# Optimization experiments

Measured on AMD Instinct MI355X. Metric: run time of the kernel, lower is better.

Reference implementation:

```python
import jax, jax.numpy as jnp
import numpy as np
from jax import lax

B, T, H, L, V = 64, 512, 1024, 4, 32000


def setup_inputs() -> dict:
    key = jax.random.key(0)
    ks = jax.random.split(key, 8)
    lengths = jax.random.randint(ks[0], (B,), T // 2, T + 1)
    tok = jax.random.randint(ks[1], (B, T), 1, V)  # valid tokens are >0; 0 is pad
    x = jnp.where(jnp.arange(T)[None, :] < lengths[:, None], tok, 0)
    s = float(1.0 / np.sqrt(H))  # torch LSTMCell default init bound
    emb = jax.random.normal(ks[2], (V, H), jnp.float32) * 0.02
    W_ih = jax.random.uniform(ks[3], (L, 4 * H, H), jnp.float32, -s, s)
    W_hh = jax.random.uniform(ks[4], (L, 4 * H, H), jnp.float32, -s, s)
    b_ih = jax.random.uniform(ks[5], (L, 4 * H), jnp.float32, -s, s)
    b_hh = jax.random.uniform(ks[6], (L, 4 * H), jnp.float32, -s, s)
    h0 = jnp.zeros((L, B, H), jnp.float32)
    c0 = jnp.zeros((L, B, H), jnp.float32)
    return {"x": x, "h0": h0, "c0": c0, "emb": emb,
            "W_ih": W_ih, "W_hh": W_hh, "b_ih": b_ih, "b_hh": b_hh}


def _lstm_stack_step(h, c, xt, W_ih, W_hh, b_ih, b_hh):
    # h, c: [L, B, H]; xt: [B, H]. Every layer is H->H (module quirk).
    inp = xt
    new_h, new_c = [], []
    for l in range(L):
        gates = inp @ W_ih[l].T + b_ih[l] + h[l] @ W_hh[l].T + b_hh[l]  # [B, 4H]
        i, f, g, o = jnp.split(gates, 4, axis=-1)  # torch gate order i,f,g,o
        i = jax.nn.sigmoid(i)
        f = jax.nn.sigmoid(f)
        g = jnp.tanh(g)
        o = jax.nn.sigmoid(o)
        cl = f * c[l] + i * g
        hl = o * jnp.tanh(cl)
        new_h.append(hl)
        new_c.append(cl)
        inp = hl
    return jnp.stack(new_h), jnp.stack(new_c)


def reference(x, h0, c0, emb, W_ih, W_hh, b_ih, b_hh):
    # lengths from pad-token convention (pad id = 0)
    lengths = jnp.sum(x > 0, axis=1)  # [B]
    # pack(..., enforce_sorted=False): sort sequences by length, descending.
    order = jnp.argsort(-lengths)          # stable descending sort
    inv = jnp.argsort(order)               # to unsort the padded output
    xs = x[order]                          # [B, T] sorted order
    lens = lengths[order]                  # [B]
    e = emb[xs]                            # [B, T, H] embedded
    mask = jnp.arange(T)[None, :] < lens[:, None]  # [B, T] active-at-step

    def step(carry, inp):
        h, c = carry                       # [L, B, H] each
        xt, m = inp                        # xt: [B, H], m: [B] bool
        nh, nc = _lstm_stack_step(h, c, xt, W_ih, W_hh, b_ih, b_hh)
        m3 = m[None, :, None]
        h2 = jnp.where(m3, nh, h)          # only active (prefix) rows advance
        c2 = jnp.where(m3, nc, c)
        out = jnp.where(m[:, None], nh[L - 1], 0.0)  # unpack zero-pads
        return (h2, c2), out

    (hF, cF), outs = lax.scan(step, (h0, c0),
                              (jnp.swapaxes(e, 0, 1), mask.T))  # scan over T
    output = jnp.swapaxes(outs, 0, 1)[inv]  # [B, T, H] back to original order
    # NOTE: the torch module returns `state` indexed in SORTED order (it never
    # unsorts the state buffer); we reproduce that quirk faithfully.
    return output, hF, cF
```

## Files before the change

### kernel.cpp

```cpp
#include <hip/hip_runtime.h>
#include <hip/hip_bf16.h>
#include <stdint.h>

#define Bn 64
#define Tn 512
#define Hn 1024
#define Ln 4
#define GN 4096
#define NDIAG (Tn + Ln - 1)

typedef __attribute__((ext_vector_type(8))) short bf16x8;
typedef __attribute__((ext_vector_type(4))) float f32x4;
typedef __attribute__((ext_vector_type(4))) unsigned short u16x4;

__device__ __forceinline__ unsigned short f2bf(float f) {
  union { float f; unsigned u; } v; v.f = f;
  return (unsigned short)((v.u + 0x7FFFu + ((v.u >> 16) & 1u)) >> 16);
}

__device__ __forceinline__ void gload16(const void* g, void* l) {
  __builtin_amdgcn_global_load_lds((const __attribute__((address_space(1))) void*)g,
                                   (__attribute__((address_space(3))) void*)l, 16, 0, 0);
}
__device__ __forceinline__ void gload16c(const void* g, void* l) {
  __builtin_amdgcn_global_load_lds((const __attribute__((address_space(1))) void*)g,
                                   (__attribute__((address_space(3))) void*)l, 16, 0, 17);
}

__device__ __forceinline__ float sigmf(float x) { return 1.0f / (1.0f + expf(-x)); }

__global__ __launch_bounds__(256) void prep_kernel(const int* __restrict__ x, int* __restrict__ len,
                                                   int* __restrict__ rank, int* __restrict__ arrive,
                                                   int* __restrict__ gen) {
  __shared__ int sl[Bn];
  int t = threadIdx.x;
  arrive[t] = 0;
  if (t == 0) *gen = 0;
  if (t < Bn) {
    int cnt = 0;
    const int* row = x + (size_t)t * Tn;
    for (int i = 0; i < Tn; ++i) cnt += (row[i] > 0) ? 1 : 0;
    sl[t] = cnt;
  }
  __syncthreads();
  if (t < Bn) {
    int Lb = sl[t], r = 0;
    for (int j = 0; j < Bn; ++j) {
      int lj = sl[j];
      r += ((lj > Lb) || (lj == Lb && j < t)) ? 1 : 0;
    }
    len[t] = Lb;
    rank[t] = r;
  }
}

__global__ void bias_kernel(const float* __restrict__ bih, const float* __restrict__ bhh,
                            float* __restrict__ bias) {
  int i = blockIdx.x * blockDim.x + threadIdx.x;
  if (i < Ln * GN) bias[i] = bih[i] + bhh[i];
}

__global__ __launch_bounds__(256) void cast_w_kernel(const float* __restrict__ Wih,
                                                     const float* __restrict__ Whh,
                                                     unsigned short* __restrict__ Wlay) {
  size_t i = (size_t)blockIdx.x * blockDim.x + threadIdx.x;
  int k4 = (int)(i & 511);
  int n  = (int)((i >> 9) & 4095);
  int l  = (int)(i >> 21);
  int bn = n >> 6, j = n & 63;
  int strip = j >> 4, hcl = j & 15;
  int g = strip * 1024 + bn * 16 + hcl;
  int k = k4 * 4;
  f32x4 v;
  if (k < 1024) v = *(const f32x4*)(Wih + ((size_t)l * GN + g) * Hn + k);
  else          v = *(const f32x4*)(Whh + ((size_t)l * GN + g) * Hn + (k - 1024));
  u16x4 pv;
#pragma unroll
  for (int u = 0; u < 4; ++u) pv[u] = f2bf(v[u]);
  *(u16x4*)(Wlay + i * 4) = pv;
}

__global__ __launch_bounds__(256) void embed_kernel(const int* __restrict__ x,
                                                    const float* __restrict__ emb,
                                                    unsigned short* __restrict__ Xemb) {
  int row = blockIdx.x;
  int t = row >> 6, b = row & 63;
  int tok = x[(size_t)b * Tn + t];
  f32x4 v = ((const f32x4*)(emb + (size_t)tok * Hn))[threadIdx.x];
  u16x4 p;
#pragma unroll
  for (int u = 0; u < 4; ++u) p[u] = f2bf(v[u]);
  ((u16x4*)(Xemb + (size_t)row * Hn))[threadIdx.x] = p;
}

__global__ __launch_bounds__(256) void init_hmask_kernel(const float* __restrict__ h0,
                                                         unsigned short* __restrict__ hmask) {
  int i = blockIdx.x * blockDim.x + threadIdx.x;
  unsigned short us = f2bf(h0[i]);
  hmask[i] = us;
  hmask[Ln * Bn * Hn + i] = us;
}

__device__ __forceinline__ void stage_chunk(const char* base, int p, char* lbuf, int tid, bool coh) {
#pragma unroll
  for (int j = 0; j < 2; ++j) {
    int o = j * 8192 + tid * 16;
    int row = o >> 8, win = o & 255;
    const char* src = base + (size_t)row * 2048 + p * 256 + (win ^ ((row & 7) << 4));
    if (coh) gload16c(src, lbuf + o);
    else     gload16(src, lbuf + o);
  }
}

__global__ __launch_bounds__(512, 2) void wavefront_kernel(
    const char* __restrict__ Wlay, const float* __restrict__ biasF,
    const char* __restrict__ Xemb,
    unsigned short* __restrict__ hmask, unsigned short* __restrict__ hfresh,
    const int* __restrict__ len, const int* __restrict__ rankp,
    const float* __restrict__ h0, const float* __restrict__ c0,
    float* __restrict__ outp, float* __restrict__ hF, float* __restrict__ cF,
    int* __restrict__ arrive, int* __restrict__ gen) {
  __shared__ char smem[65536];
  int tid = threadIdx.x, bid = blockIdx.x;
  int cell = (bid & 7) >> 1;
  int bn = (bid & 1) * 32 + (bid >> 3);
  int w = tid >> 6, lane = tid & 63, l15 = lane & 15, lk = lane >> 4;
  int kh = w >> 2, s = w & 3;

  bf16x8 wreg[32];
  {
    const char* wrow = Wlay + ((size_t)((cell * 64 + bn) * 64 + s * 16 + l15)) * 4096
                       + kh * 2048 + lk * 16;
#pragma unroll
    for (int i = 0; i < 32; ++i)
      wreg[i] = *(const bf16x8*)(wrow + i * 64);
  }

  int r = tid >> 2;
  int c0i = (tid & 3) << 2;
  int hc = bn * 16 + c0i;
  f32x4 bI = {}, bF = {}, bG = {}, bO = {}, hold = {}, cold = {};
  int lenr = 0, rnkr = 0;
  if (tid < 256) {
    const float* bias = biasF + cell * GN;
    bI = *(const f32x4*)(bias + hc);
    bF = *(const f32x4*)(bias + 1024 + hc);
    bG = *(const f32x4*)(bias + 2048 + hc);
    bO = *(const f32x4*)(bias + 3072 + hc);
    lenr = len[r];
    rnkr = rankp[r];
    hold = *(const f32x4*)(h0 + ((size_t)cell * Bn + r) * Hn + hc);
    cold = *(const f32x4*)(c0 + ((size_t)cell * Bn + r) * Hn + hc);
  }

  for (int d = 0; d < NDIAG; ++d) {
    int t = d - cell;
    if (t >= 0 && t < Tn) {
      int p = d & 1;
      bool cohLo = (cell != 0);
      const char* inbase = (cell == 0)
          ? (Xemb + (size_t)t * (Bn * Hn * 2))
          : (const char*)(hfresh + ((size_t)p * Ln + (cell - 1)) * (Bn * Hn));
      const char* hmbase = (const char*)(hmask + ((size_t)p * Ln + cell) * (Bn * Hn));
      unsigned short* hmW = hmask + ((size_t)(p ^ 1) * Ln + cell) * (Bn * Hn);
      unsigned short* hfW = hfresh + ((size_t)(p ^ 1) * Ln + cell) * (Bn * Hn);

      f32x4 acc[4] = {};
      stage_chunk(inbase, 0, smem + 0 * 16384, tid, cohLo);
      stage_chunk(hmbase, 0, smem + 2 * 16384, tid, true);
#pragma unroll
      for (int ph = 0; ph < 8; ++ph) {
        __syncthreads();
        if (ph < 7) {
          int par = (ph + 1) & 1;
          stage_chunk(inbase, ph + 1, smem + (0 * 2 + par) * 16384, tid, cohLo);
          stage_chunk(hmbase, ph + 1, smem + (1 * 2 + par) * 16384, tid, true);
        }
        const char* lb = smem + (kh * 2 + (ph & 1)) * 16384;
#pragma unroll
        for (int ksl = 0; ksl < 4; ++ksl) {
#pragma unroll
          for (int mi = 0; mi < 4; ++mi) {
            int row = mi * 16 + l15;
            bf16x8 afr = *(const bf16x8*)(lb + row * 256 + ((ksl * 64 + lk * 16) ^ ((row & 7) << 4)));
            acc[mi] = __builtin_amdgcn_mfma_f32_16x16x32_bf16(afr, wreg[ph * 4 + ksl],
                                                              acc[mi], 0, 0, 0);
          }
        }
      }

      float* ex = (float*)smem + kh * 8192 + s * 1024;
#pragma unroll
      for (int mi = 0; mi < 4; ++mi)
#pragma unroll
        for (int j = 0; j < 4; ++j)
          ex[(mi * 16 + lk * 4 + j) * 16 + l15] = acc[mi][j];
      __syncthreads();

      if (tid < 256) {
        float* smf = (float*)smem;
        f32x4 sI = *(const f32x4*)(smf + r * 16 + c0i)        + *(const f32x4*)(smf + 8192 + r * 16 + c0i);
        f32x4 sF = *(const f32x4*)(smf + 1024 + r * 16 + c0i) + *(const f32x4*)(smf + 9216 + r * 16 + c0i);
        f32x4 sG = *(const f32x4*)(smf + 2048 + r * 16 + c0i) + *(const f32x4*)(smf + 10240 + r * 16 + c0i);
        f32x4 sO = *(const f32x4*)(smf + 3072 + r * 16 + c0i) + *(const f32x4*)(smf + 11264 + r * 16 + c0i);
        bool msk = (t < lenr);
        f32x4 hx;
#pragma unroll
        for (int u = 0; u < 4; ++u) {
          float iv = sigmf(sI[u] + bI[u]);
          float fv = sigmf(sF[u] + bF[u]);
          float gv = tanhf(sG[u] + bG[u]);
          float ov = sigmf(sO[u] + bO[u]);
          float cc = fv * cold[u] + iv * gv;
          float hh = ov * tanhf(cc);
          hx[u] = hh;
          cold[u] = msk ? cc : cold[u];
          hold[u] = msk ? hh : hold[u];
        }
        unsigned hb01 = (unsigned)f2bf(hold[0]) | ((unsigned)f2bf(hold[1]) << 16);
        unsigned hb23 = (unsigned)f2bf(hold[2]) | ((unsigned)f2bf(hold[3]) << 16);
        unsigned xb01 = (unsigned)f2bf(hx[0]) | ((unsigned)f2bf(hx[1]) << 16);
        unsigned xb23 = (unsigned)f2bf(hx[2]) | ((unsigned)f2bf(hx[3]) << 16);
        unsigned* hm32 = (unsigned*)(hmW + (size_t)r * Hn + hc);
        unsigned* hf32p = (unsigned*)(hfW + (size_t)r * Hn + hc);
        __hip_atomic_store(hm32,     hb01, __ATOMIC_RELAXED, __HIP_MEMORY_SCOPE_AGENT);
        __hip_atomic_store(hm32 + 1, hb23, __ATOMIC_RELAXED, __HIP_MEMORY_SCOPE_AGENT);
        __hip_atomic_store(hf32p,     xb01, __ATOMIC_RELAXED, __HIP_MEMORY_SCOPE_AGENT);
        __hip_atomic_store(hf32p + 1, xb23, __ATOMIC_RELAXED, __HIP_MEMORY_SCOPE_AGENT);
        if (cell == Ln - 1) {
          f32x4 o4;
#pragma unroll
          for (int u = 0; u < 4; ++u) o4[u] = msk ? hx[u] : 0.0f;
          *(f32x4*)(outp + ((size_t)r * Tn + t) * Hn + hc) = o4;
        }
      }
    }

    __syncthreads();
    if (tid == 0)
      __hip_atomic_store(&arrive[bid], d + 1, __ATOMIC_RELAXED, __HIP_MEMORY_SCOPE_AGENT);
    if (bid == 0) {
      if (tid < 256) {
        while (__hip_atomic_load(&arrive[tid], __ATOMIC_RELAXED, __HIP_MEMORY_SCOPE_AGENT) <= d)
          __builtin_amdgcn_s_sleep(1);
      }
      __syncthreads();
      if (tid == 0)
        __hip_atomic_store(gen, d + 1, __ATOMIC_RELAXED, __HIP_MEMORY_SCOPE_AGENT);
    } else {
      if (tid == 0) {
        while (__hip_atomic_load(gen, __ATOMIC_RELAXED, __HIP_MEMORY_SCOPE_AGENT) <= d)
          __builtin_amdgcn_s_sleep(1);
      }
      __syncthreads();
    }
    asm volatile("" ::: "memory");
  }

  if (tid < 256) {
    *(f32x4*)(hF + ((size_t)cell * Bn + rnkr) * Hn + hc) = hold;
    *(f32x4*)(cF + ((size_t)cell * Bn + rnkr) * Hn + hc) = cold;
  }
}

extern "C" void kernel_launch(void* const* d_in, const int* in_sizes, int n_in,
                              void* d_out, int out_size, void* d_ws, size_t ws_size,
                              hipStream_t stream) {
  const int*   x   = (const int*)d_in[0];
  const float* h0  = (const float*)d_in[1];
  const float* c0  = (const float*)d_in[2];
  const float* emb = (const float*)d_in[3];
  const float* Wih = (const float*)d_in[4];
  const float* Whh = (const float*)d_in[5];
  const float* bih = (const float*)d_in[6];
  const float* bhh = (const float*)d_in[7];
  float* out = (float*)d_out;

  char* ws = (char*)d_ws;
  unsigned short* Wlay  = (unsigned short*)ws;
  float*          biasF = (float*)(ws + 67108864);
  unsigned short* Xemb  = (unsigned short*)(ws + 67174400);
  unsigned short* hmask = (unsigned short*)(ws + 134283264);
  unsigned short* hfresh= (unsigned short*)(ws + 135331840);
  int*            leni  = (int*)(ws + 136380416);
  int*            ranki = (int*)(ws + 136380672);
  int*            arrv  = (int*)(ws + 136380928);
  int*            genp  = (int*)(ws + 136381952);

  prep_kernel<<<1, 256, 0, stream>>>(x, leni, ranki, arrv, genp);
  bias_kernel<<<64, 256, 0, stream>>>(bih, bhh, biasF);
  cast_w_kernel<<<32768, 256, 0, stream>>>(Wih, Whh, Wlay);
  embed_kernel<<<Tn * Bn, 256, 0, stream>>>(x, emb, Xemb);
  init_hmask_kernel<<<1024, 256, 0, stream>>>(h0, hmask);

  float* hFbase = out + (size_t)Bn * Tn * Hn;
  float* cFbase = hFbase + (size_t)Ln * Bn * Hn;

  wavefront_kernel<<<256, 512, 0, stream>>>(
      (const char*)Wlay, biasF, (const char*)Xemb, hmask, hfresh,
      leni, ranki, h0, c0, out, hFbase, cFbase, arrv, genp);
}
```

Before: 4.833 ms.

## Replace global grid barrier with per-layer counters and deepen staging pipeline

Drops the all-block barrier that ran after every diagonal and uses per-layer arrival counters instead. Each block waits only on the previous layer, its own layer, and the layer after it two steps back. The hmask/hfresh buffers become four-deep so layers can run up to two diagonals apart. The K-loop now uses a three-stage LDS ring with explicit vmcnt waits, a new wave split (4 K-quarters x 2 gate-slice pairs) and a 16-row swizzle. This adds LDS usage (96KB) and a 16-way reduction in return for less grid-wide synchronisation stall.

```diff
diff --git a/kernel.cpp b/kernel.cpp
--- a/kernel.cpp
+++ b/kernel.cpp
@@ -8,6 +8,7 @@
 #define Ln 4
 #define GN 4096
 #define NDIAG (Tn + Ln - 1)
+#define LBH (Ln * Bn * Hn)
 
 typedef __attribute__((ext_vector_type(8))) short bf16x8;
 typedef __attribute__((ext_vector_type(4))) float f32x4;
@@ -30,12 +31,10 @@
 __device__ __forceinline__ float sigmf(float x) { return 1.0f / (1.0f + expf(-x)); }
 
 __global__ __launch_bounds__(256) void prep_kernel(const int* __restrict__ x, int* __restrict__ len,
-                                                   int* __restrict__ rank, int* __restrict__ arrive,
-                                                   int* __restrict__ gen) {
+                                                   int* __restrict__ rank, int* __restrict__ arr) {
   __shared__ int sl[Bn];
   int t = threadIdx.x;
-  arrive[t] = 0;
-  if (t == 0) *gen = 0;
+  if (t < 4) arr[t] = 0;
   if (t < Bn) {
     int cnt = 0;
     const int* row = x + (size_t)t * Tn;
@@ -97,18 +96,22 @@
                                                          unsigned short* __restrict__ hmask) {
   int i = blockIdx.x * blockDim.x + threadIdx.x;
   unsigned short us = f2bf(h0[i]);
-  hmask[i] = us;
-  hmask[Ln * Bn * Hn + i] = us;
-}
-
-__device__ __forceinline__ void stage_chunk(const char* base, int p, char* lbuf, int tid, bool coh) {
+#pragma unroll
+  for (int dep = 0; dep < 4; ++dep)
+    hmask[(size_t)dep * LBH + i] = us;
+}
+
+__device__ __forceinline__ void stage2(const char* inb, const char* hmb, int ph, char* buf,
+                                       int tid, bool cohIn) {
 #pragma unroll
   for (int j = 0; j < 2; ++j) {
     int o = j * 8192 + tid * 16;
     int row = o >> 8, win = o & 255;
-    const char* src = base + (size_t)row * 2048 + p * 256 + (win ^ ((row & 7) << 4));
-    if (coh) gload16c(src, lbuf + o);
-    else     gload16(src, lbuf + o);
+    int sw = win ^ ((row & 15) << 4);
+    const char* s1 = inb + (size_t)row * 2048 + ph * 256 + sw;
+    if (cohIn) gload16c(s1, buf + o);
+    else       gload16(s1, buf + o);
+    gload16c(hmb + (size_t)row * 2048 + ph * 256 + sw, buf + 16384 + o);
   }
 }
 
@@ -119,21 +122,24 @@
     const int* __restrict__ len, const int* __restrict__ rankp,
     const float* __restrict__ h0, const float* __restrict__ c0,
     float* __restrict__ outp, float* __restrict__ hF, float* __restrict__ cF,
-    int* __restrict__ arrive, int* __restrict__ gen) {
-  __shared__ char smem[65536];
+    int* __restrict__ arr) {
+  __shared__ char smem[98304];
   int tid = threadIdx.x, bid = blockIdx.x;
   int cell = (bid & 7) >> 1;
   int bn = (bid & 1) * 32 + (bid >> 3);
   int w = tid >> 6, lane = tid & 63, l15 = lane & 15, lk = lane >> 4;
-  int kh = w >> 2, s = w & 3;
+  int kq = w >> 1, sp = w & 1;
 
   bf16x8 wreg[32];
-  {
-    const char* wrow = Wlay + ((size_t)((cell * 64 + bn) * 64 + s * 16 + l15)) * 4096
-                       + kh * 2048 + lk * 16;
-#pragma unroll
-    for (int i = 0; i < 32; ++i)
-      wreg[i] = *(const bf16x8*)(wrow + i * 64);
+#pragma unroll
+  for (int st = 0; st < 2; ++st) {
+    const char* wr = Wlay + ((size_t)((cell * 64 + bn) * 64 + (sp * 2 + st) * 16 + l15)) * 4096
+                   + (kq >= 2 ? 2048 : 0) + (kq & 1) * 128 + lk * 16;
+#pragma unroll
+    for (int ph = 0; ph < 8; ++ph)
+#pragma unroll
+      for (int j = 0; j < 2; ++j)
+        wreg[st * 16 + ph * 2 + j] = *(const bf16x8*)(wr + ph * 256 + j * 64);
   }
 
   int r = tid >> 2;
@@ -156,61 +162,92 @@
   for (int d = 0; d < NDIAG; ++d) {
     int t = d - cell;
     if (t >= 0 && t < Tn) {
-      int p = d & 1;
-      bool cohLo = (cell != 0);
+      if (tid == 0 && cell > 0) {
+        int thr = 64 * d;
+        while (__hip_atomic_load(&arr[cell - 1], __ATOMIC_RELAXED, __HIP_MEMORY_SCOPE_AGENT) < thr)
+          __builtin_amdgcn_s_sleep(1);
+      }
+      if (tid == 1) {
+        int thr = 64 * d;
+        while (__hip_atomic_load(&arr[cell], __ATOMIC_RELAXED, __HIP_MEMORY_SCOPE_AGENT) < thr)
+          __builtin_amdgcn_s_sleep(1);
+      }
+      if (tid == 2 && cell < Ln - 1 && d >= 2) {
+        int thr = 64 * (d - 2);
+        while (__hip_atomic_load(&arr[cell + 1], __ATOMIC_RELAXED, __HIP_MEMORY_SCOPE_AGENT) < thr)
+          __builtin_amdgcn_s_sleep(1);
+      }
+      __syncthreads();
+
+      bool cohIn = (cell != 0);
       const char* inbase = (cell == 0)
           ? (Xemb + (size_t)t * (Bn * Hn * 2))
-          : (const char*)(hfresh + ((size_t)p * Ln + (cell - 1)) * (Bn * Hn));
-      const char* hmbase = (const char*)(hmask + ((size_t)p * Ln + cell) * (Bn * Hn));
-      unsigned short* hmW = hmask + ((size_t)(p ^ 1) * Ln + cell) * (Bn * Hn);
-      unsigned short* hfW = hfresh + ((size_t)(p ^ 1) * Ln + cell) * (Bn * Hn);
-
-      f32x4 acc[4] = {};
-      stage_chunk(inbase, 0, smem + 0 * 16384, tid, cohLo);
-      stage_chunk(hmbase, 0, smem + 2 * 16384, tid, true);
+          : (const char*)(hfresh + ((size_t)((d - 1) & 3) * Ln + (cell - 1)) * (Bn * Hn));
+      const char* hmbase = (const char*)(hmask + ((size_t)((d - 1) & 3) * Ln + cell) * (Bn * Hn));
+      unsigned short* hmW = hmask + ((size_t)(d & 3) * Ln + cell) * (Bn * Hn);
+      unsigned short* hfW = hfresh + ((size_t)(d & 3) * Ln + cell) * (Bn * Hn);
+
+      f32x4 acc[2][4] = {};
+      stage2(inbase, hmbase, 0, smem, tid, cohIn);
+      stage2(inbase, hmbase, 1, smem + 32768, tid, cohIn);
 #pragma unroll
       for (int ph = 0; ph < 8; ++ph) {
-        __syncthreads();
-        if (ph < 7) {
-          int par = (ph + 1) & 1;
-          stage_chunk(inbase, ph + 1, smem + (0 * 2 + par) * 16384, tid, cohLo);
-          stage_chunk(hmbase, ph + 1, smem + (1 * 2 + par) * 16384, tid, true);
-        }
-        const char* lb = smem + (kh * 2 + (ph & 1)) * 16384;
-#pragma unroll
-        for (int ksl = 0; ksl < 4; ++ksl) {
+        if (ph < 7) asm volatile("s_waitcnt vmcnt(4)" ::: "memory");
+        else        asm volatile("s_waitcnt vmcnt(0)" ::: "memory");
+        __builtin_amdgcn_s_barrier();
+        if (ph < 6) stage2(inbase, hmbase, ph + 2, smem + ((ph + 2) % 3) * 32768, tid, cohIn);
+        const char* chunk = smem + (ph % 3) * 32768 + (kq >= 2 ? 16384 : 0);
+        int colb = (kq & 1) * 128;
+#pragma unroll
+        for (int j = 0; j < 2; ++j) {
 #pragma unroll
           for (int mi = 0; mi < 4; ++mi) {
             int row = mi * 16 + l15;
-            bf16x8 afr = *(const bf16x8*)(lb + row * 256 + ((ksl * 64 + lk * 16) ^ ((row & 7) << 4)));
-            acc[mi] = __builtin_amdgcn_mfma_f32_16x16x32_bf16(afr, wreg[ph * 4 + ksl],
-                                                              acc[mi], 0, 0, 0);
+            bf16x8 afr = *(const bf16x8*)(chunk + row * 256 +
+                          ((colb + j * 64 + lk * 16) ^ ((row & 15) << 4)));
+            acc[0][mi] = __builtin_amdgcn_mfma_f32_16x16x32_bf16(afr, wreg[ph * 2 + j],
+                                                                 acc[0][mi], 0, 0, 0);
+            acc[1][mi] = __builtin_amdgcn_mfma_f32_16x16x32_bf16(afr, wreg[16 + ph * 2 + j],
+                                                                 acc[1][mi], 0, 0, 0);
           }
         }
       }
 
-      float* ex = (float*)smem + kh * 8192 + s * 1024;
-#pragma unroll
-      for (int mi = 0; mi < 4; ++mi)
-#pragma unroll
-        for (int j = 0; j < 4; ++j)
-          ex[(mi * 16 + lk * 4 + j) * 16 + l15] = acc[mi][j];
+#pragma unroll
+      for (int st = 0; st < 2; ++st) {
+        int ri = kq * 4 + (sp * 2 + st);
+        float* exf = (float*)(smem + (ri < 8 ? ri * 4096 : 32768 + ri * 4096));
+#pragma unroll
+        for (int mi = 0; mi < 4; ++mi)
+#pragma unroll
+          for (int j = 0; j < 4; ++j)
+            exf[(mi * 16 + lk * 4 + j) * 16 + l15] = acc[st][mi][j];
+      }
       __syncthreads();
 
       if (tid < 256) {
-        float* smf = (float*)smem;
-        f32x4 sI = *(const f32x4*)(smf + r * 16 + c0i)        + *(const f32x4*)(smf + 8192 + r * 16 + c0i);
-        f32x4 sF = *(const f32x4*)(smf + 1024 + r * 16 + c0i) + *(const f32x4*)(smf + 9216 + r * 16 + c0i);
-        f32x4 sG = *(const f32x4*)(smf + 2048 + r * 16 + c0i) + *(const f32x4*)(smf + 10240 + r * 16 + c0i);
-        f32x4 sO = *(const f32x4*)(smf + 3072 + r * 16 + c0i) + *(const f32x4*)(smf + 11264 + r * 16 + c0i);
+        f32x4 sv[4];
+#pragma unroll
+        for (int g = 0; g < 4; ++g) {
+          f32x4 s = {};
+#pragma unroll
+          for (int q = 0; q < 4; ++q) {
+            int ri = q * 4 + g;
+            const float* exf = (const float*)(smem + (ri < 8 ? ri * 4096 : 32768 + ri * 4096));
+            f32x4 v = *(const f32x4*)(exf + r * 16 + c0i);
+#pragma unroll
+            for (int u = 0; u < 4; ++u) s[u] += v[u];
+          }
+          sv[g] = s;
+        }
         bool msk = (t < lenr);
         f32x4 hx;
 #pragma unroll
         for (int u = 0; u < 4; ++u) {
-          float iv = sigmf(sI[u] + bI[u]);
-          float fv = sigmf(sF[u] + bF[u]);
-          float gv = tanhf(sG[u] + bG[u]);
-          float ov = sigmf(sO[u] + bO[u]);
+          float iv = sigmf(sv[0][u] + bI[u]);
+          float fv = sigmf(sv[1][u] + bF[u]);
+          float gv = tanhf(sv[2][u] + bG[u]);
+          float ov = sigmf(sv[3][u] + bO[u]);
           float cc = fv * cold[u] + iv * gv;
           float hh = ov * tanhf(cc);
           hx[u] = hh;
@@ -238,23 +275,7 @@
 
     __syncthreads();
     if (tid == 0)
-      __hip_atomic_store(&arrive[bid], d + 1, __ATOMIC_RELAXED, __HIP_MEMORY_SCOPE_AGENT);
-    if (bid == 0) {
-      if (tid < 256) {
-        while (__hip_atomic_load(&arrive[tid], __ATOMIC_RELAXED, __HIP_MEMORY_SCOPE_AGENT) <= d)
-          __builtin_amdgcn_s_sleep(1);
-      }
-      __syncthreads();
-      if (tid == 0)
-        __hip_atomic_store(gen, d + 1, __ATOMIC_RELAXED, __HIP_MEMORY_SCOPE_AGENT);
-    } else {
-      if (tid == 0) {
-        while (__hip_atomic_load(gen, __ATOMIC_RELAXED, __HIP_MEMORY_SCOPE_AGENT) <= d)
-          __builtin_amdgcn_s_sleep(1);
-      }
-      __syncthreads();
-    }
-    asm volatile("" ::: "memory");
+      __hip_atomic_fetch_add(&arr[cell], 1, __ATOMIC_RELAXED, __HIP_MEMORY_SCOPE_AGENT);
   }
 
   if (tid < 256) {
@@ -281,13 +302,12 @@
   float*          biasF = (float*)(ws + 67108864);
   unsigned short* Xemb  = (unsigned short*)(ws + 67174400);
   unsigned short* hmask = (unsigned short*)(ws + 134283264);
-  unsigned short* hfresh= (unsigned short*)(ws + 135331840);
-  int*            leni  = (int*)(ws + 136380416);
-  int*            ranki = (int*)(ws + 136380672);
-  int*            arrv  = (int*)(ws + 136380928);
-  int*            genp  = (int*)(ws + 136381952);
-
-  prep_kernel<<<1, 256, 0, stream>>>(x, leni, ranki, arrv, genp);
+  unsigned short* hfresh= (unsigned short*)(ws + 136380416);
+  int*            leni  = (int*)(ws + 138477568);
+  int*            ranki = (int*)(ws + 138477824);
+  int*            arrp  = (int*)(ws + 138478080);
+
+  prep_kernel<<<1, 256, 0, stream>>>(x, leni, ranki, arrp);
   bias_kernel<<<64, 256, 0, stream>>>(bih, bhh, biasF);
   cast_w_kernel<<<32768, 256, 0, stream>>>(Wih, Whh, Wlay);
   embed_kernel<<<Tn * Bn, 256, 0, stream>>>(x, emb, Xemb);
@@ -298,5 +318,5 @@
 
   wavefront_kernel<<<256, 512, 0, stream>>>(
       (const char*)Wlay, biasF, (const char*)Xemb, hmask, hfresh,
-      leni, ranki, h0, c0, out, hFbase, cFbase, arrv, genp);
-}
+      leni, ranki, h0, c0, out, hFbase, cFbase, arrp);
+}
```

After: 5.629 ms. +16.5%, slower.

## Split LSTM cells into input/recurrent blocks with per-slot flag dataflow sync

Applied to the files above, without the earlier changes.

Replaces the global grid barrier per diagonal with fine-grained per-slot flag polling. Each layer is split into separate input-projection blocks (W_ih) and recurrent blocks (W_hh). Input blocks publish partial gate sums through a ring buffer in global memory, so the input projection can run ahead of the recurrence. Weights are converted to bf16 straight into registers inside the kernel, which removes the separate cast kernel. The change adds global traffic for the partials, uses deeper ring buffers and a larger LDS footprint, and relies on bounded polling that could deadlock or time out if blocks are not co-resident.

```diff
diff --git a/kernel.cpp b/kernel.cpp
--- a/kernel.cpp
+++ b/kernel.cpp
@@ -7,35 +7,50 @@
 #define Hn 1024
 #define Ln 4
 #define GN 4096
-#define NDIAG (Tn + Ln - 1)
+#define POLL_CAP 2000000
 
 typedef __attribute__((ext_vector_type(8))) short bf16x8;
 typedef __attribute__((ext_vector_type(4))) float f32x4;
 typedef __attribute__((ext_vector_type(4))) unsigned short u16x4;
+typedef unsigned long long u64t;
 
 __device__ __forceinline__ unsigned short f2bf(float f) {
   union { float f; unsigned u; } v; v.f = f;
   return (unsigned short)((v.u + 0x7FFFu + ((v.u >> 16) & 1u)) >> 16);
 }
 
-__device__ __forceinline__ void gload16(const void* g, void* l) {
+template<int AUX>
+__device__ __forceinline__ void gloadT(const void* g, void* l) {
   __builtin_amdgcn_global_load_lds((const __attribute__((address_space(1))) void*)g,
-                                   (__attribute__((address_space(3))) void*)l, 16, 0, 0);
-}
-__device__ __forceinline__ void gload16c(const void* g, void* l) {
-  __builtin_amdgcn_global_load_lds((const __attribute__((address_space(1))) void*)g,
-                                   (__attribute__((address_space(3))) void*)l, 16, 0, 17);
+                                   (__attribute__((address_space(3))) void*)l, 16, 0, AUX);
+}
+
+__device__ __forceinline__ int aload(const int* p) {
+  return __hip_atomic_load(p, __ATOMIC_RELAXED, __HIP_MEMORY_SCOPE_AGENT);
 }
 
 __device__ __forceinline__ float sigmf(float x) { return 1.0f / (1.0f + expf(-x)); }
 
+template<int AUX>
+__device__ __forceinline__ void stageChunk(const char* base, int ph, char* buf, int tid) {
+#pragma unroll
+  for (int j = 0; j < 4; ++j) {
+    int o = j * 8192 + tid * 16;
+    int row = o >> 9, win = o & 511;
+    gloadT<AUX>(base + (size_t)row * 2048 + ph * 512 + (win ^ ((row & 15) << 4)), buf + o);
+  }
+}
+__device__ __forceinline__ void stageAny(int coh, const char* base, int ph, char* buf, int tid) {
+  if (coh) stageChunk<17>(base, ph, buf, tid);
+  else     stageChunk<0>(base, ph, buf, tid);
+}
+
 __global__ __launch_bounds__(256) void prep_kernel(const int* __restrict__ x, int* __restrict__ len,
-                                                   int* __restrict__ rank, int* __restrict__ arrive,
-                                                   int* __restrict__ gen) {
+                                                   int* __restrict__ rank, int* __restrict__ flags) {
   __shared__ int sl[Bn];
   int t = threadIdx.x;
-  arrive[t] = 0;
-  if (t == 0) *gen = 0;
+#pragma unroll
+  for (int k = 0; k < 4; ++k) flags[t + 256 * k] = 0;
   if (t < Bn) {
     int cnt = 0;
     const int* row = x + (size_t)t * Tn;
@@ -58,26 +73,6 @@
                             float* __restrict__ bias) {
   int i = blockIdx.x * blockDim.x + threadIdx.x;
   if (i < Ln * GN) bias[i] = bih[i] + bhh[i];
-}
-
-__global__ __launch_bounds__(256) void cast_w_kernel(const float* __restrict__ Wih,
-                                                     const float* __restrict__ Whh,
-                                                     unsigned short* __restrict__ Wlay) {
-  size_t i = (size_t)blockIdx.x * blockDim.x + threadIdx.x;
-  int k4 = (int)(i & 511);
-  int n  = (int)((i >> 9) & 4095);
-  int l  = (int)(i >> 21);
-  int bn = n >> 6, j = n & 63;
-  int strip = j >> 4, hcl = j & 15;
-  int g = strip * 1024 + bn * 16 + hcl;
-  int k = k4 * 4;
-  f32x4 v;
-  if (k < 1024) v = *(const f32x4*)(Wih + ((size_t)l * GN + g) * Hn + k);
-  else          v = *(const f32x4*)(Whh + ((size_t)l * GN + g) * Hn + (k - 1024));
-  u16x4 pv;
-#pragma unroll
-  for (int u = 0; u < 4; ++u) pv[u] = f2bf(v[u]);
-  *(u16x4*)(Wlay + i * 4) = pv;
 }
 
 __global__ __launch_bounds__(256) void embed_kernel(const int* __restrict__ x,
@@ -94,172 +89,203 @@
 }
 
 __global__ __launch_bounds__(256) void init_hmask_kernel(const float* __restrict__ h0,
-                                                         unsigned short* __restrict__ hmask) {
+                                                         unsigned short* __restrict__ hmaskB) {
   int i = blockIdx.x * blockDim.x + threadIdx.x;
-  unsigned short us = f2bf(h0[i]);
-  hmask[i] = us;
-  hmask[Ln * Bn * Hn + i] = us;
-}
-
-__device__ __forceinline__ void stage_chunk(const char* base, int p, char* lbuf, int tid, bool coh) {
-#pragma unroll
-  for (int j = 0; j < 2; ++j) {
-    int o = j * 8192 + tid * 16;
-    int row = o >> 8, win = o & 255;
-    const char* src = base + (size_t)row * 2048 + p * 256 + (win ^ ((row & 7) << 4));
-    if (coh) gload16c(src, lbuf + o);
-    else     gload16(src, lbuf + o);
-  }
+  int c = i >> 16, rem = i & 65535;
+  hmaskB[(size_t)(c * 4 + 3) * 65536 + rem] = f2bf(h0[i]);
 }
 
 __global__ __launch_bounds__(512, 2) void wavefront_kernel(
-    const char* __restrict__ Wlay, const float* __restrict__ biasF,
-    const char* __restrict__ Xemb,
-    unsigned short* __restrict__ hmask, unsigned short* __restrict__ hfresh,
-    const int* __restrict__ len, const int* __restrict__ rankp,
+    const float* __restrict__ Wih, const float* __restrict__ Whh,
+    const float* __restrict__ biasF, const char* __restrict__ Xemb,
+    unsigned short* __restrict__ hmaskB, unsigned short* __restrict__ hfresh,
+    float* __restrict__ part, const int* __restrict__ len, const int* __restrict__ rankp,
     const float* __restrict__ h0, const float* __restrict__ c0,
     float* __restrict__ outp, float* __restrict__ hF, float* __restrict__ cF,
-    int* __restrict__ arrive, int* __restrict__ gen) {
-  __shared__ char smem[65536];
+    int* __restrict__ flags) {
+  __shared__ char smem[131072];
   int tid = threadIdx.x, bid = blockIdx.x;
-  int cell = (bid & 7) >> 1;
-  int bn = (bid & 1) * 32 + (bid >> 3);
-  int w = tid >> 6, lane = tid & 63, l15 = lane & 15, lk = lane >> 4;
-  int kh = w >> 2, s = w & 3;
-
-  bf16x8 wreg[32];
-  {
-    const char* wrow = Wlay + ((size_t)((cell * 64 + bn) * 64 + s * 16 + l15)) * 4096
-                       + kh * 2048 + lk * 16;
-#pragma unroll
-    for (int i = 0; i < 32; ++i)
-      wreg[i] = *(const bf16x8*)(wrow + i * 64);
-  }
-
-  int r = tid >> 2;
-  int c0i = (tid & 3) << 2;
-  int hc = bn * 16 + c0i;
-  f32x4 bI = {}, bF = {}, bG = {}, bO = {}, hold = {}, cold = {};
+  int grp = bid & 7;
+  int isH = (grp < 4) ? 1 : 0;
+  int cell = grp & 3, slot = bid >> 3;
+  int sp = tid >> 6, lane = tid & 63, l15 = lane & 15, lk = lane >> 4;
+  int* hfarr = flags;
+  int* xparr = flags + 128;
+
+  int j = sp * 16 + l15;
+  const float* wrow = (isH ? Whh : Wih) + (size_t)cell * GN * Hn
+                    + (size_t)((j >> 5) * 1024 + slot * 32 + (j & 31)) * Hn + lk * 8;
+  bf16x8 a0,a1,a2,a3,a4,a5,a6,a7,a8,a9,a10,a11,a12,a13,a14,a15;
+  bf16x8 b0,b1,b2,b3,b4,b5,b6,b7,b8,b9,b10,b11,b12,b13,b14,b15;
+#define LW(R, I) { f32x4 u0_ = *(const f32x4*)(wrow + (I) * 32);                         \
+    f32x4 u1_ = *(const f32x4*)(wrow + (I) * 32 + 4); bf16x8 t_;                          \
+    t_[0]=(short)f2bf(u0_[0]); t_[1]=(short)f2bf(u0_[1]); t_[2]=(short)f2bf(u0_[2]);      \
+    t_[3]=(short)f2bf(u0_[3]); t_[4]=(short)f2bf(u1_[0]); t_[5]=(short)f2bf(u1_[1]);      \
+    t_[6]=(short)f2bf(u1_[2]); t_[7]=(short)f2bf(u1_[3]); R = t_; }
+  LW(a0,0)  LW(a1,1)  LW(a2,2)  LW(a3,3)  LW(a4,4)  LW(a5,5)  LW(a6,6)  LW(a7,7)
+  LW(a8,8)  LW(a9,9)  LW(a10,10) LW(a11,11) LW(a12,12) LW(a13,13) LW(a14,14) LW(a15,15)
+  LW(b0,16) LW(b1,17) LW(b2,18) LW(b3,19) LW(b4,20) LW(b5,21) LW(b6,22) LW(b7,23)
+  LW(b8,24) LW(b9,25) LW(b10,26) LW(b11,27) LW(b12,28) LW(b13,29) LW(b14,30) LW(b15,31)
+#undef LW
+
+  int r = tid >> 3, hcl = (tid & 7) * 4;
+  int hcg = slot * 32 + hcl;
+  f32x4 bIv = {}, bFv = {}, bGv = {}, bOv = {}, hold = {}, cold = {};
   int lenr = 0, rnkr = 0;
-  if (tid < 256) {
+  if (isH) {
     const float* bias = biasF + cell * GN;
-    bI = *(const f32x4*)(bias + hc);
-    bF = *(const f32x4*)(bias + 1024 + hc);
-    bG = *(const f32x4*)(bias + 2048 + hc);
-    bO = *(const f32x4*)(bias + 3072 + hc);
-    lenr = len[r];
-    rnkr = rankp[r];
-    hold = *(const f32x4*)(h0 + ((size_t)cell * Bn + r) * Hn + hc);
-    cold = *(const f32x4*)(c0 + ((size_t)cell * Bn + r) * Hn + hc);
-  }
-
-  for (int d = 0; d < NDIAG; ++d) {
-    int t = d - cell;
-    if (t >= 0 && t < Tn) {
-      int p = d & 1;
-      bool cohLo = (cell != 0);
-      const char* inbase = (cell == 0)
-          ? (Xemb + (size_t)t * (Bn * Hn * 2))
-          : (const char*)(hfresh + ((size_t)p * Ln + (cell - 1)) * (Bn * Hn));
-      const char* hmbase = (const char*)(hmask + ((size_t)p * Ln + cell) * (Bn * Hn));
-      unsigned short* hmW = hmask + ((size_t)(p ^ 1) * Ln + cell) * (Bn * Hn);
-      unsigned short* hfW = hfresh + ((size_t)(p ^ 1) * Ln + cell) * (Bn * Hn);
-
-      f32x4 acc[4] = {};
-      stage_chunk(inbase, 0, smem + 0 * 16384, tid, cohLo);
-      stage_chunk(hmbase, 0, smem + 2 * 16384, tid, true);
-#pragma unroll
-      for (int ph = 0; ph < 8; ++ph) {
-        __syncthreads();
-        if (ph < 7) {
-          int par = (ph + 1) & 1;
-          stage_chunk(inbase, ph + 1, smem + (0 * 2 + par) * 16384, tid, cohLo);
-          stage_chunk(hmbase, ph + 1, smem + (1 * 2 + par) * 16384, tid, true);
-        }
-        const char* lb = smem + (kh * 2 + (ph & 1)) * 16384;
-#pragma unroll
-        for (int ksl = 0; ksl < 4; ++ksl) {
-#pragma unroll
-          for (int mi = 0; mi < 4; ++mi) {
-            int row = mi * 16 + l15;
-            bf16x8 afr = *(const bf16x8*)(lb + row * 256 + ((ksl * 64 + lk * 16) ^ ((row & 7) << 4)));
-            acc[mi] = __builtin_amdgcn_mfma_f32_16x16x32_bf16(afr, wreg[ph * 4 + ksl],
-                                                              acc[mi], 0, 0, 0);
-          }
-        }
+    bIv = *(const f32x4*)(bias + hcg);
+    bFv = *(const f32x4*)(bias + 1024 + hcg);
+    bGv = *(const f32x4*)(bias + 2048 + hcg);
+    bOv = *(const f32x4*)(bias + 3072 + hcg);
+    lenr = len[r]; rnkr = rankp[r];
+    hold = *(const f32x4*)(h0 + ((size_t)cell * Bn + r) * Hn + hcg);
+    cold = *(const f32x4*)(c0 + ((size_t)cell * Bn + r) * Hn + hcg);
+  }
+
+#define PHASE(P, VMSTR, NEXT, R0,R1,R2,R3,R4,R5,R6,R7)                                    \
+  {                                                                                       \
+    asm volatile("s_waitcnt " VMSTR ::: "memory");                                        \
+    __builtin_amdgcn_s_barrier();                                                         \
+    if ((NEXT) >= 0) stageAny(coh, inb, (NEXT), smem + ((NEXT) % 3) * 32768, tid);        \
+    const char* chunk_ = smem + ((P) % 3) * 32768;                                        \
+    _Pragma("unroll")                                                                     \
+    for (int ks_ = 0; ks_ < 8; ++ks_) {                                                   \
+      int kb_ = ks_ * 64 + lk * 16;                                                       \
+      bf16x8 wv_ = (ks_==0?R0:ks_==1?R1:ks_==2?R2:ks_==3?R3:ks_==4?R4:ks_==5?R5:ks_==6?R6:R7); \
+      _Pragma("unroll")                                                                   \
+      for (int mi_ = 0; mi_ < 4; ++mi_) {                                                 \
+        int row_ = mi_ * 16 + l15;                                                        \
+        bf16x8 af_ = *(const bf16x8*)(chunk_ + row_ * 512 + (kb_ ^ ((row_ & 15) << 4)));  \
+        acc[mi_] = __builtin_amdgcn_mfma_f32_16x16x32_bf16(af_, wv_, acc[mi_], 0, 0, 0);  \
+      }                                                                                   \
+    }                                                                                     \
+  }
+
+#define POLLALL(PTR_EXPR, THR)                                                            \
+  for (int it_ = 0; it_ < POLL_CAP; ++it_) {                                              \
+    int v_ = aload(PTR_EXPR);                                                             \
+    if (__all(v_ >= (THR))) break;                                                        \
+    __builtin_amdgcn_s_sleep(1);                                                          \
+  }
+#define POLLONE(PTR, THR)                                                                 \
+  for (int it_ = 0; it_ < POLL_CAP; ++it_) {                                              \
+    if (aload(PTR) >= (THR)) break;                                                       \
+    __builtin_amdgcn_s_sleep(1);                                                          \
+  }
+
+  for (int t = 0; t < Tn; ++t) {
+    if (isH) {
+      if (sp == 0) { POLLALL(&hfarr[cell * 32 + (lane & 31)], t) }
+      if (sp == 1 && lane == 0) { POLLONE(&xparr[cell * 32 + slot], t + 1) }
+      if (sp == 2 && cell < 3) { POLLALL(&xparr[(cell + 1) * 32 + (lane & 31)], t - 7) }
+    } else {
+      if (sp == 0 && cell > 0) { POLLALL(&hfarr[(cell - 1) * 32 + (lane & 31)], t + 1) }
+      if (sp == 1 && lane == 0) { POLLONE(&hfarr[cell * 32 + slot], t - 3) }
+    }
+    __syncthreads();
+
+    const char* inb;
+    int coh;
+    if (isH) {
+      inb = (const char*)hmaskB + (size_t)(cell * 4 + ((t - 1) & 3)) * 131072;  coh = 1;
+    } else if (cell == 0) {
+      inb = Xemb + (size_t)t * 131072;  coh = 0;
+    } else {
+      inb = (const char*)hfresh + (size_t)((cell - 1) * 8 + (t & 7)) * 131072;  coh = 1;
+    }
+
+    if (isH) {
+      const char* psrc = (const char*)part + (size_t)((cell * 4 + (t & 3)) * 32 + slot) * 32768;
+#pragma unroll
+      for (int jj = 0; jj < 4; ++jj) {
+        int o = jj * 8192 + tid * 16;
+        gloadT<17>(psrc + o, smem + 98304 + o);
       }
-
-      float* ex = (float*)smem + kh * 8192 + s * 1024;
+    }
+    stageAny(coh, inb, 0, smem, tid);
+    stageAny(coh, inb, 1, smem + 32768, tid);
+
+    f32x4 acc[4] = {};
+    PHASE(0, "vmcnt(4)", 2, a0,a1,a2,a3,a4,a5,a6,a7)
+    PHASE(1, "vmcnt(4)", 3, a8,a9,a10,a11,a12,a13,a14,a15)
+    PHASE(2, "vmcnt(4)", -1, b0,b1,b2,b3,b4,b5,b6,b7)
+    PHASE(3, "vmcnt(0)", -1, b8,b9,b10,b11,b12,b13,b14,b15)
+
+    {
+      float* ex = (float*)(smem + 32768) + sp * 1024;
 #pragma unroll
       for (int mi = 0; mi < 4; ++mi)
 #pragma unroll
-        for (int j = 0; j < 4; ++j)
-          ex[(mi * 16 + lk * 4 + j) * 16 + l15] = acc[mi][j];
-      __syncthreads();
-
-      if (tid < 256) {
-        float* smf = (float*)smem;
-        f32x4 sI = *(const f32x4*)(smf + r * 16 + c0i)        + *(const f32x4*)(smf + 8192 + r * 16 + c0i);
-        f32x4 sF = *(const f32x4*)(smf + 1024 + r * 16 + c0i) + *(const f32x4*)(smf + 9216 + r * 16 + c0i);
-        f32x4 sG = *(const f32x4*)(smf + 2048 + r * 16 + c0i) + *(const f32x4*)(smf + 10240 + r * 16 + c0i);
-        f32x4 sO = *(const f32x4*)(smf + 3072 + r * 16 + c0i) + *(const f32x4*)(smf + 11264 + r * 16 + c0i);
-        bool msk = (t < lenr);
-        f32x4 hx;
-#pragma unroll
-        for (int u = 0; u < 4; ++u) {
-          float iv = sigmf(sI[u] + bI[u]);
-          float fv = sigmf(sF[u] + bF[u]);
-          float gv = tanhf(sG[u] + bG[u]);
-          float ov = sigmf(sO[u] + bO[u]);
-          float cc = fv * cold[u] + iv * gv;
-          float hh = ov * tanhf(cc);
-          hx[u] = hh;
-          cold[u] = msk ? cc : cold[u];
-          hold[u] = msk ? hh : hold[u];
-        }
-        unsigned hb01 = (unsigned)f2bf(hold[0]) | ((unsigned)f2bf(hold[1]) << 16);
-        unsigned hb23 = (unsigned)f2bf(hold[2]) | ((unsigned)f2bf(hold[3]) << 16);
-        unsigned xb01 = (unsigned)f2bf(hx[0]) | ((unsigned)f2bf(hx[1]) << 16);
-        unsigned xb23 = (unsigned)f2bf(hx[2]) | ((unsigned)f2bf(hx[3]) << 16);
-        unsigned* hm32 = (unsigned*)(hmW + (size_t)r * Hn + hc);
-        unsigned* hf32p = (unsigned*)(hfW + (size_t)r * Hn + hc);
-        __hip_atomic_store(hm32,     hb01, __ATOMIC_RELAXED, __HIP_MEMORY_SCOPE_AGENT);
-        __hip_atomic_store(hm32 + 1, hb23, __ATOMIC_RELAXED, __HIP_MEMORY_SCOPE_AGENT);
-        __hip_atomic_store(hf32p,     xb01, __ATOMIC_RELAXED, __HIP_MEMORY_SCOPE_AGENT);
-        __hip_atomic_store(hf32p + 1, xb23, __ATOMIC_RELAXED, __HIP_MEMORY_SCOPE_AGENT);
-        if (cell == Ln - 1) {
-          f32x4 o4;
-#pragma unroll
-          for (int u = 0; u < 4; ++u) o4[u] = msk ? hx[u] : 0.0f;
-          *(f32x4*)(outp + ((size_t)r * Tn + t) * Hn + hc) = o4;
-        }
+        for (int jj = 0; jj < 4; ++jj)
+          ex[(mi * 16 + lk * 4 + jj) * 16 + l15] = acc[mi][jj];
+    }
+    __syncthreads();
+
+    if (isH) {
+      const float* exf = (const float*)(smem + 32768);
+      const float* pf  = (const float*)(smem + 98304);
+      f32x4 g4[4];
+#pragma unroll
+      for (int g = 0; g < 4; ++g) {
+        int off = (g * 2 + (hcl >> 4)) * 1024 + r * 16 + (hcl & 15);
+        f32x4 e = *(const f32x4*)(exf + off);
+        f32x4 p = *(const f32x4*)(pf + off);
+#pragma unroll
+        for (int u = 0; u < 4; ++u) g4[g][u] = e[u] + p[u];
       }
-    }
-
-    __syncthreads();
-    if (tid == 0)
-      __hip_atomic_store(&arrive[bid], d + 1, __ATOMIC_RELAXED, __HIP_MEMORY_SCOPE_AGENT);
-    if (bid == 0) {
-      if (tid < 256) {
-        while (__hip_atomic_load(&arrive[tid], __ATOMIC_RELAXED, __HIP_MEMORY_SCOPE_AGENT) <= d)
-          __builtin_amdgcn_s_sleep(1);
+      bool msk = (t < lenr);
+      f32x4 hx;
+#pragma unroll
+      for (int u = 0; u < 4; ++u) {
+        float iv = sigmf(g4[0][u] + bIv[u]);
+        float fv = sigmf(g4[1][u] + bFv[u]);
+        float gv = tanhf(g4[2][u] + bGv[u]);
+        float ov = sigmf(g4[3][u] + bOv[u]);
+        float cc = fv * cold[u] + iv * gv;
+        float hh = ov * tanhf(cc);
+        hx[u] = hh;
+        cold[u] = msk ? cc : cold[u];
+        hold[u] = msk ? hh : hold[u];
+      }
+      u64t hb64 = (u64t)f2bf(hold[0]) | ((u64t)f2bf(hold[1]) << 16)
+                | ((u64t)f2bf(hold[2]) << 32) | ((u64t)f2bf(hold[3]) << 48);
+      u64t xb64 = (u64t)f2bf(hx[0]) | ((u64t)f2bf(hx[1]) << 16)
+                | ((u64t)f2bf(hx[2]) << 32) | ((u64t)f2bf(hx[3]) << 48);
+      u64t* hmW = (u64t*)(hmaskB + (size_t)(cell * 4 + (t & 3)) * 65536 + (size_t)r * Hn + hcg);
+      u64t* hfW = (u64t*)(hfresh + (size_t)(cell * 8 + (t & 7)) * 65536 + (size_t)r * Hn + hcg);
+      __hip_atomic_store(hmW, hb64, __ATOMIC_RELAXED, __HIP_MEMORY_SCOPE_AGENT);
+      __hip_atomic_store(hfW, xb64, __ATOMIC_RELAXED, __HIP_MEMORY_SCOPE_AGENT);
+      if (cell == 3) {
+        f32x4 o4;
+#pragma unroll
+        for (int u = 0; u < 4; ++u) o4[u] = msk ? hx[u] : 0.0f;
+        *(f32x4*)(outp + ((size_t)r * Tn + t) * Hn + hcg) = o4;
       }
       __syncthreads();
       if (tid == 0)
-        __hip_atomic_store(gen, d + 1, __ATOMIC_RELAXED, __HIP_MEMORY_SCOPE_AGENT);
+        __hip_atomic_store(&hfarr[cell * 32 + slot], t + 1, __ATOMIC_RELAXED,
+                           __HIP_MEMORY_SCOPE_AGENT);
     } else {
-      if (tid == 0) {
-        while (__hip_atomic_load(gen, __ATOMIC_RELAXED, __HIP_MEMORY_SCOPE_AGENT) <= d)
-          __builtin_amdgcn_s_sleep(1);
-      }
+      float* pdst = part + (size_t)((cell * 4 + (t & 3)) * 32 + slot) * 8192;
+      const u64t* src = (const u64t*)(smem + 32768) + tid * 8;
+      u64t* dst = (u64t*)pdst + tid * 8;
+#pragma unroll
+      for (int ii = 0; ii < 8; ++ii)
+        __hip_atomic_store(&dst[ii], src[ii], __ATOMIC_RELAXED, __HIP_MEMORY_SCOPE_AGENT);
       __syncthreads();
-    }
-    asm volatile("" ::: "memory");
-  }
-
-  if (tid < 256) {
-    *(f32x4*)(hF + ((size_t)cell * Bn + rnkr) * Hn + hc) = hold;
-    *(f32x4*)(cF + ((size_t)cell * Bn + rnkr) * Hn + hc) = cold;
+      if (tid == 0)
+        __hip_atomic_store(&xparr[cell * 32 + slot], t + 1, __ATOMIC_RELAXED,
+                           __HIP_MEMORY_SCOPE_AGENT);
+    }
+  }
+#undef PHASE
+#undef POLLALL
+#undef POLLONE
+
+  if (isH) {
+    *(f32x4*)(hF + ((size_t)cell * Bn + rnkr) * Hn + hcg) = hold;
+    *(f32x4*)(cF + ((size_t)cell * Bn + rnkr) * Hn + hcg) = cold;
   }
 }
 
@@ -277,26 +303,24 @@
   float* out = (float*)d_out;
 
   char* ws = (char*)d_ws;
-  unsigned short* Wlay  = (unsigned short*)ws;
-  float*          biasF = (float*)(ws + 67108864);
-  unsigned short* Xemb  = (unsigned short*)(ws + 67174400);
-  unsigned short* hmask = (unsigned short*)(ws + 134283264);
-  unsigned short* hfresh= (unsigned short*)(ws + 135331840);
-  int*            leni  = (int*)(ws + 136380416);
-  int*            ranki = (int*)(ws + 136380672);
-  int*            arrv  = (int*)(ws + 136380928);
-  int*            genp  = (int*)(ws + 136381952);
-
-  prep_kernel<<<1, 256, 0, stream>>>(x, leni, ranki, arrv, genp);
+  unsigned short* Xemb   = (unsigned short*)ws;
+  float*          part   = (float*)(ws + 67108864);
+  unsigned short* hmaskB = (unsigned short*)(ws + 83886080);
+  unsigned short* hfresh = (unsigned short*)(ws + 85983232);
+  float*          biasF  = (float*)(ws + 90177536);
+  int*            leni   = (int*)(ws + 90243072);
+  int*            ranki  = (int*)(ws + 90243328);
+  int*            flags  = (int*)(ws + 90243584);
+
+  prep_kernel<<<1, 256, 0, stream>>>(x, leni, ranki, flags);
   bias_kernel<<<64, 256, 0, stream>>>(bih, bhh, biasF);
-  cast_w_kernel<<<32768, 256, 0, stream>>>(Wih, Whh, Wlay);
   embed_kernel<<<Tn * Bn, 256, 0, stream>>>(x, emb, Xemb);
-  init_hmask_kernel<<<1024, 256, 0, stream>>>(h0, hmask);
+  init_hmask_kernel<<<1024, 256, 0, stream>>>(h0, hmaskB);
 
   float* hFbase = out + (size_t)Bn * Tn * Hn;
   float* cFbase = hFbase + (size_t)Ln * Bn * Hn;
 
   wavefront_kernel<<<256, 512, 0, stream>>>(
-      (const char*)Wlay, biasF, (const char*)Xemb, hmask, hfresh,
-      leni, ranki, h0, c0, out, hFbase, cFbase, arrv, genp);
-}
+      Wih, Whh, biasF, (const char*)Xemb, hmaskB, hfresh, part,
+      leni, ranki, h0, c0, out, hFbase, cFbase, flags);
+}
```

Measured after the change: 7.003 ms. +44.9%, slower.
